# Optimization experiments

Measured on AMD Instinct MI355X. Metric: run time of the kernel, lower is better.

The kernel has to match this reference:

```python
import jax, jax.numpy as jnp
import numpy as np

N_LINKS = 10000
N_PATHS = 50000
PLEN = 5                 # fixed path length -> max_len
E = N_PATHS * PLEN       # number of (link, path) edge entries
D = 32                   # link_state_dim == path_state_dim
H = 32
RU = 256                 # readout_units
T_ITERS = 8              # message-passing iterations t


def setup_inputs() -> dict:
    key = jax.random.key(0)
    ks = jax.random.split(key, 20)
    s = 0.1
    inp = {}
    inp["traffic"] = jax.random.uniform(ks[0], (N_PATHS,), dtype=jnp.float32)
    inp["packets"] = jax.random.uniform(ks[1], (N_PATHS,), dtype=jnp.float32)
    inp["time_dist_params"] = jax.random.normal(ks[2], (N_PATHS, 12), dtype=jnp.float32)
    inp["capacity"] = jax.random.uniform(ks[3], (N_LINKS,), dtype=jnp.float32)
    # edge lists: each path has exactly PLEN links
    inp["link_to_path"] = jax.random.randint(ks[4], (E,), 0, N_LINKS, dtype=jnp.int32)
    inp["path_ids"] = jnp.repeat(jnp.arange(N_PATHS, dtype=jnp.int32), PLEN)
    inp["sequence_path"] = jnp.tile(jnp.arange(PLEN, dtype=jnp.int32), N_PATHS)
    inp["path_to_link"] = jax.random.randint(ks[5], (E,), 0, N_PATHS, dtype=jnp.int32)
    inp["sequence_links"] = jax.random.randint(ks[6], (E,), 0, N_LINKS, dtype=jnp.int32)
    inp["n_links"] = N_LINKS
    inp["n_paths"] = N_PATHS
    # path-update GRU (input D -> hidden H), torch layout [3H, in]
    inp["Wi_p"] = jax.random.normal(ks[7], (3 * H, D), dtype=jnp.float32) * s
    inp["Wh_p"] = jax.random.normal(ks[8], (3 * H, H), dtype=jnp.float32) * s
    inp["bi_p"] = jnp.zeros((3 * H,), jnp.float32)
    inp["bh_p"] = jnp.zeros((3 * H,), jnp.float32)
    # link-update GRUCell (input H -> hidden D)
    inp["Wi_l"] = jax.random.normal(ks[9], (3 * D, H), dtype=jnp.float32) * s
    inp["Wh_l"] = jax.random.normal(ks[10], (3 * D, D), dtype=jnp.float32) * s
    inp["bi_l"] = jnp.zeros((3 * D,), jnp.float32)
    inp["bh_l"] = jnp.zeros((3 * D,), jnp.float32)
    # readout MLP
    inp["W1"] = jax.random.normal(ks[11], (RU, H), dtype=jnp.float32) * s
    inp["b1"] = jnp.zeros((RU,), jnp.float32)
    inp["W2"] = jax.random.normal(ks[12], (RU, RU), dtype=jnp.float32) * s
    inp["b2"] = jnp.zeros((RU,), jnp.float32)
    inp["W3"] = jax.random.normal(ks[13], (1, RU), dtype=jnp.float32) * s
    inp["b3"] = jnp.zeros((1,), jnp.float32)
    return inp


def _gru_step(x, h, Wi, Wh, bi, bh):
    # torch GRU gate math
    gi = x @ Wi.T + bi
    gh = h @ Wh.T + bh
    ir, iz, in_ = jnp.split(gi, 3, axis=-1)
    hr, hz, hn = jnp.split(gh, 3, axis=-1)
    r = jax.nn.sigmoid(ir + hr)
    z = jax.nn.sigmoid(iz + hz)
    n = jnp.tanh(in_ + r * hn)
    return (1.0 - z) * n + z * h


def reference(traffic, packets, time_dist_params, capacity,
              link_to_path, path_ids, sequence_path, path_to_link, sequence_links,
              n_links, n_paths,
              Wi_p, Wh_p, bi_p, bh_p, Wi_l, Wh_l, bi_l, bh_l,
              W1, b1, W2, b2, W3, b3):
    max_len = PLEN  # == sequence_path.max() + 1 (static)
    # per-path valid lengths (equivalent to the torch nonzero-row count loop)
    lens = jax.ops.segment_max(sequence_path, path_ids, num_segments=n_paths) + 1
    link_state = jnp.concatenate(
        [capacity[:, None], jnp.zeros((n_links, D - 1), capacity.dtype)], axis=1)
    path_state = jnp.concatenate(
        [traffic[:, None], packets[:, None], time_dist_params,
         jnp.zeros((n_paths, D - 14), traffic.dtype)], axis=1)

    for _ in range(T_ITERS):
        link_gather = link_state[link_to_path]  # [E, D]
        link_inputs = jnp.zeros((n_paths, max_len, D), link_state.dtype)
        link_inputs = link_inputs.at[path_ids, sequence_path].set(link_gather)

        def step(h, xt_t):
            xt, t = xt_t
            h_new = _gru_step(xt, h, Wi_p, Wh_p, bi_p, bh_p)
            h = jnp.where((t < lens)[:, None], h_new, h)  # pack_padded semantics
            return h, None

        path_state, _ = jax.lax.scan(
            step, path_state,
            (jnp.swapaxes(link_inputs, 0, 1), jnp.arange(max_len)))

        path_gather = path_state[path_to_link]  # [E, H]
        path_sum = jnp.zeros((n_links, H), path_gather.dtype).at[sequence_links].add(path_gather)
        link_state = _gru_step(path_sum, link_state, Wi_l, Wh_l, bi_l, bh_l)

    r = jax.nn.relu(path_state @ W1.T + b1)
    r = jax.nn.relu(r @ W2.T + b2)
    r = r @ W3.T + b3            # [n_paths, 1]
    return r[:, 0][None, :]      # [1, n_paths]
```

## Files before the change

### kernel.cpp

```cpp
#include <hip/hip_runtime.h>

#define NP 50000
#define NL 10000
#define PLEN 5
#define NE (NP * PLEN)
#define DD 32
#define RUU 256
#define TITERS 8
#define PPW 8

__device__ __forceinline__ float sigmoidf_(float a) {
    return 1.0f / (1.0f + __expf(-a));
}
__device__ __forceinline__ float tanhf_(float a) {
    a = fminf(fmaxf(a, -15.0f), 15.0f);
    float t = __expf(2.0f * a);
    return (t - 1.0f) / (t + 1.0f);
}

__global__ __launch_bounds__(256) void k_init(
    const float* __restrict__ traffic, const float* __restrict__ packets,
    const float* __restrict__ tdp, const float* __restrict__ capacity,
    float* __restrict__ path_state, float* __restrict__ link_state,
    int* __restrict__ lens, int* __restrict__ cnt) {
    int i = blockIdx.x * 256 + threadIdx.x;
    if (i < NP) {
        float v[DD];
        v[0] = traffic[i];
        v[1] = packets[i];
#pragma unroll
        for (int k = 0; k < 12; k++) v[2 + k] = tdp[i * 12 + k];
#pragma unroll
        for (int k = 14; k < DD; k++) v[k] = 0.0f;
#pragma unroll
        for (int k = 0; k < DD; k++) path_state[i * DD + k] = v[k];
        lens[i] = 0;
    }
    if (i < NL) {
        link_state[i * DD] = capacity[i];
#pragma unroll
        for (int k = 1; k < DD; k++) link_state[i * DD + k] = 0.0f;
        cnt[i] = 0;
    }
}

__global__ __launch_bounds__(256) void k_lens(const int* __restrict__ path_ids,
                                              const int* __restrict__ seq_path,
                                              int* __restrict__ lens) {
    int e = blockIdx.x * 256 + threadIdx.x;
    if (e < NE) atomicMax(&lens[path_ids[e]], seq_path[e] + 1);
}

__global__ __launch_bounds__(256) void k_csr_count(const int* __restrict__ seq_links,
                                                   int* __restrict__ cnt) {
    int e = blockIdx.x * 256 + threadIdx.x;
    if (e < NE) atomicAdd(&cnt[seq_links[e]], 1);
}

__global__ __launch_bounds__(256) void k_csr_scan(const int* __restrict__ cnt,
                                                  int* __restrict__ offs,
                                                  int* __restrict__ cursor) {
    __shared__ int ssum[256];
    const int tid = threadIdx.x;
    const int CH = 40;
    int base = tid * CH;
    int s = 0;
    for (int i = 0; i < CH; i++) {
        int idx = base + i;
        s += (idx < NL) ? cnt[idx] : 0;
    }
    ssum[tid] = s;
    __syncthreads();
    for (int off = 1; off < 256; off <<= 1) {
        int t = (tid >= off) ? ssum[tid - off] : 0;
        __syncthreads();
        ssum[tid] += t;
        __syncthreads();
    }
    int run = ssum[tid] - s;
    for (int i = 0; i < CH; i++) {
        int idx = base + i;
        if (idx < NL) {
            offs[idx] = run;
            cursor[idx] = run;
            run += cnt[idx];
        }
    }
    if (tid == 0) offs[NL] = ssum[255];
}

__global__ __launch_bounds__(256) void k_csr_fill(const int* __restrict__ seq_links,
                                                  const int* __restrict__ path_to_link,
                                                  int* __restrict__ cursor,
                                                  int* __restrict__ csr_pids) {
    int e = blockIdx.x * 256 + threadIdx.x;
    if (e < NE) {
        int l = seq_links[e];
        int slot = atomicAdd(&cursor[l], 1);
        csr_pids[slot] = path_to_link[e];
    }
}

__global__ __launch_bounds__(256, 2) void k_gru_paths(
    const float* __restrict__ link_state, float* __restrict__ path_state,
    const int* __restrict__ link_to_path, const int* __restrict__ lens,
    const float* __restrict__ Wi, const float* __restrict__ Wh,
    const float* __restrict__ bi, const float* __restrict__ bh) {
    __shared__ float hbuf[4][DD];
    const int tid = threadIdx.x;
    const int wave = tid >> 6;
    const int lane = tid & 63;
    const int d = lane & 31;
    const int half = lane >> 5;

    float wi[3][16], wh[3][16];
#pragma unroll
    for (int g = 0; g < 3; g++) {
        const float* wip = &Wi[(g * 32 + d) * 32 + half * 16];
        const float* whp = &Wh[(g * 32 + d) * 32 + half * 16];
#pragma unroll
        for (int c = 0; c < 4; c++) {
            *(float4*)&wi[g][c * 4] = *(const float4*)&wip[c * 4];
            *(float4*)&wh[g][c * 4] = *(const float4*)&whp[c * 4];
        }
    }
#pragma unroll
    for (int g = 0; g < 3; g++)
#pragma unroll
        for (int k = 0; k < 16; k++) {
            asm volatile("" : "+v"(wi[g][k]));
            asm volatile("" : "+v"(wh[g][k]));
        }
    const float bir = bi[d], biz = bi[d + 32], bin = bi[d + 64];
    const float bhr = bh[d], bhz = bh[d + 32], bhn = bh[d + 64];

    const int pbase = (blockIdx.x * 4 + wave) * PPW;
    for (int pp = 0; pp < PPW; pp++) {
        const int p = pbase + pp;
        if (p >= NP) break;

        float hd = path_state[p * DD + d];
        float hk[16];
#pragma unroll
        for (int c = 0; c < 4; c++)
            *(float4*)&hk[c * 4] = *(const float4*)&path_state[p * DD + half * 16 + c * 4];

        const int len = lens[p];
        int li[PLEN];
#pragma unroll
        for (int s = 0; s < PLEN; s++) li[s] = link_to_path[p * PLEN + s];

        float xk[16];
#pragma unroll
        for (int c = 0; c < 4; c++)
            *(float4*)&xk[c * 4] = *(const float4*)&link_state[li[0] * DD + half * 16 + c * 4];

#pragma unroll
        for (int st = 0; st < PLEN; st++) {
            float xn[16];
            if (st + 1 < PLEN) {
#pragma unroll
                for (int c = 0; c < 4; c++)
                    *(float4*)&xn[c * 4] =
                        *(const float4*)&link_state[li[st + 1] * DD + half * 16 + c * 4];
            }
            float ir = 0.f, iz = 0.f, in_ = 0.f, hr = 0.f, hz = 0.f, hn = 0.f;
#pragma unroll
            for (int k = 0; k < 16; k++) {
                ir  = fmaf(xk[k], wi[0][k], ir);
                iz  = fmaf(xk[k], wi[1][k], iz);
                in_ = fmaf(xk[k], wi[2][k], in_);
                hr  = fmaf(hk[k], wh[0][k], hr);
                hz  = fmaf(hk[k], wh[1][k], hz);
                hn  = fmaf(hk[k], wh[2][k], hn);
            }
            ir += __shfl_xor(ir, 32);
            iz += __shfl_xor(iz, 32);
            in_ += __shfl_xor(in_, 32);
            hr += __shfl_xor(hr, 32);
            hz += __shfl_xor(hz, 32);
            hn += __shfl_xor(hn, 32);
            float r = sigmoidf_(ir + bir + hr + bhr);
            float z = sigmoidf_(iz + biz + hz + bhz);
            float n = tanhf_(in_ + bin + r * (hn + bhn));
            float hnew = (1.0f - z) * n + z * hd;
            hd = (st < len) ? hnew : hd;
            hbuf[wave][d] = hd;
#pragma unroll
            for (int c = 0; c < 4; c++)
                *(float4*)&hk[c * 4] = *(const float4*)&hbuf[wave][half * 16 + c * 4];
            if (st + 1 < PLEN) {
#pragma unroll
                for (int k = 0; k < 16; k++) xk[k] = xn[k];
            }
        }
        if (half == 0) path_state[p * DD + d] = hd;
    }
}

__global__ __launch_bounds__(256, 2) void k_links(
    const float* __restrict__ path_state, float* __restrict__ link_state,
    const int* __restrict__ offs, const int* __restrict__ csr_pids,
    const float* __restrict__ Wi, const float* __restrict__ Wh,
    const float* __restrict__ bi, const float* __restrict__ bh) {
    __shared__ float hbuf[4][DD];
    const int tid = threadIdx.x;
    const int wave = tid >> 6;
    const int lane = tid & 63;
    const int d = lane & 31;
    const int half = lane >> 5;

    float wi[3][16], wh[3][16];
#pragma unroll
    for (int g = 0; g < 3; g++) {
        const float* wip = &Wi[(g * 32 + d) * 32 + half * 16];
        const float* whp = &Wh[(g * 32 + d) * 32 + half * 16];
#pragma unroll
        for (int c = 0; c < 4; c++) {
            *(float4*)&wi[g][c * 4] = *(const float4*)&wip[c * 4];
            *(float4*)&wh[g][c * 4] = *(const float4*)&whp[c * 4];
        }
    }
#pragma unroll
    for (int g = 0; g < 3; g++)
#pragma unroll
        for (int k = 0; k < 16; k++) {
            asm volatile("" : "+v"(wi[g][k]));
            asm volatile("" : "+v"(wh[g][k]));
        }
    const float bir = bi[d], biz = bi[d + 32], bin = bi[d + 64];
    const float bhr = bh[d], bhz = bh[d + 32], bhn = bh[d + 64];

    const int lbase = (blockIdx.x * 4 + wave) * PPW;
    for (int ll = 0; ll < PPW; ll++) {
        const int l = lbase + ll;
        if (l >= NL) break;
        const int beg = offs[l], end = offs[l + 1];

        float xv = 0.f;
        int t = beg + half;
        int pid = (t < end) ? csr_pids[t] : 0;
        while (t < end) {
            int t2 = t + 2;
            int pid2 = (t2 < end) ? csr_pids[t2] : 0;
            xv += path_state[pid * DD + d];
            pid = pid2;
            t = t2;
        }
        xv += __shfl_xor(xv, 32);

        float hd = link_state[l * DD + d];
        float hk[16], xk[16];
#pragma unroll
        for (int c = 0; c < 4; c++)
            *(float4*)&hk[c * 4] = *(const float4*)&link_state[l * DD + half * 16 + c * 4];
        hbuf[wave][d] = xv;
#pragma unroll
        for (int c = 0; c < 4; c++)
            *(float4*)&xk[c * 4] = *(const float4*)&hbuf[wave][half * 16 + c * 4];

        float ir = 0.f, iz = 0.f, in_ = 0.f, hr = 0.f, hz = 0.f, hn = 0.f;
#pragma unroll
        for (int k = 0; k < 16; k++) {
            ir  = fmaf(xk[k], wi[0][k], ir);
            iz  = fmaf(xk[k], wi[1][k], iz);
            in_ = fmaf(xk[k], wi[2][k], in_);
            hr  = fmaf(hk[k], wh[0][k], hr);
            hz  = fmaf(hk[k], wh[1][k], hz);
            hn  = fmaf(hk[k], wh[2][k], hn);
        }
        ir += __shfl_xor(ir, 32);
        iz += __shfl_xor(iz, 32);
        in_ += __shfl_xor(in_, 32);
        hr += __shfl_xor(hr, 32);
        hz += __shfl_xor(hz, 32);
        hn += __shfl_xor(hn, 32);
        float r = sigmoidf_(ir + bir + hr + bhr);
        float z = sigmoidf_(iz + biz + hz + bhz);
        float n = tanhf_(in_ + bin + r * (hn + bhn));
        float hnew = (1.0f - z) * n + z * hd;
        if (half == 0) link_state[l * DD + d] = hnew;
    }
}

__global__ __launch_bounds__(256, 2) void k_readout(
    const float* __restrict__ path_state, float* __restrict__ out,
    const float* __restrict__ W1, const float* __restrict__ b1,
    const float* __restrict__ W2, const float* __restrict__ b2,
    const float* __restrict__ W3, const float* __restrict__ b3) {
    __shared__ float sr1[64 * RUU];
    __shared__ float sw[RUU * 32];
    __shared__ float sred[64 * 32];
    const int tid = threadIdx.x;
    const int p0 = blockIdx.x * 64;

    {
        float4* dst = (float4*)sred;
#pragma unroll
        for (int r = 0; r < 2; r++) {
            int gidx = r * 256 + tid;
            int row = gidx >> 3, f4 = gidx & 7;
            int p = p0 + row;
            if (p >= NP) p = NP - 1;
            dst[gidx] = *(const float4*)&path_state[(size_t)p * DD + f4 * 4];
        }
    }
    float w1r[DD];
#pragma unroll
    for (int c = 0; c < 8; c++)
        *(float4*)&w1r[c * 4] = *(const float4*)&W1[tid * DD + c * 4];
    float bb1 = b1[tid];
    __syncthreads();

    for (int m = 0; m < 64; m++) {
        float acc = bb1;
        const float4* xr = (const float4*)&sred[m * DD];
#pragma unroll
        for (int c = 0; c < 8; c++) {
            float4 xv = xr[c];
            acc = fmaf(xv.x, w1r[c * 4 + 0], fmaf(xv.y, w1r[c * 4 + 1],
                  fmaf(xv.z, w1r[c * 4 + 2], fmaf(xv.w, w1r[c * 4 + 3], acc))));
        }
        sr1[m * RUU + tid] = fmaxf(acc, 0.0f);
    }

    const int pig = tid >> 5;
    const int jg  = tid & 31;
    float accs[8][8];
#pragma unroll
    for (int jj = 0; jj < 8; jj++) {
        float bv = b2[jg * 8 + jj];
#pragma unroll
        for (int pp = 0; pp < 8; pp++) accs[pp][jj] = bv;
    }
    for (int s = 0; s < 8; s++) {
        __syncthreads();
#pragma unroll
        for (int r = 0; r < 8; r++) {
            int gidx = r * 256 + tid;
            int j = gidx >> 3, kk = gidx & 7;
            float4 v = *(const float4*)&W2[j * RUU + s * 32 + kk * 4];
            ((float4*)sw)[j * 8 + (kk ^ ((j >> 3) & 7))] = v;
        }
        __syncthreads();
        for (int k4 = 0; k4 < 8; k4++) {
            float a[8][4];
#pragma unroll
            for (int pp = 0; pp < 8; pp++)
                *(float4*)&a[pp][0] =
                    *(const float4*)&sr1[(pig * 8 + pp) * RUU + s * 32 + k4 * 4];
#pragma unroll
            for (int jj = 0; jj < 8; jj++) {
                float4 w = ((const float4*)sw)[(jg * 8 + jj) * 8 + (k4 ^ (jg & 7))];
#pragma unroll
                for (int pp = 0; pp < 8; pp++) {
                    accs[pp][jj] = fmaf(a[pp][0], w.x, fmaf(a[pp][1], w.y,
                                   fmaf(a[pp][2], w.z, fmaf(a[pp][3], w.w, accs[pp][jj]))));
                }
            }
        }
    }

    float w3r[8];
#pragma unroll
    for (int c = 0; c < 2; c++)
        *(float4*)&w3r[c * 4] = *(const float4*)&W3[jg * 8 + c * 4];
#pragma unroll
    for (int pp = 0; pp < 8; pp++) {
        float v = 0.f;
#pragma unroll
        for (int jj = 0; jj < 8; jj++) v = fmaf(w3r[jj], fmaxf(accs[pp][jj], 0.f), v);
        sred[(pig * 8 + pp) * 32 + jg] = v;
    }
    __syncthreads();
    if (tid < 64) {
        float v = b3[0];
        const float* sp = &sred[tid * 32];
#pragma unroll
        for (int g = 0; g < 32; g++) v += sp[g];
        int p = p0 + tid;
        if (p < NP) out[p] = v;
    }
}

extern "C" void kernel_launch(void* const* d_in, const int* in_sizes, int n_in,
                              void* d_out, int out_size, void* d_ws, size_t ws_size,
                              hipStream_t stream) {
    const float* traffic  = (const float*)d_in[0];
    const float* packets  = (const float*)d_in[1];
    const float* tdp      = (const float*)d_in[2];
    const float* capacity = (const float*)d_in[3];
    const int* link_to_path = (const int*)d_in[4];
    const int* path_ids     = (const int*)d_in[5];
    const int* seq_path     = (const int*)d_in[6];
    const int* path_to_link = (const int*)d_in[7];
    const int* seq_links    = (const int*)d_in[8];
    const float* Wi_p = (const float*)d_in[11];
    const float* Wh_p = (const float*)d_in[12];
    const float* bi_p = (const float*)d_in[13];
    const float* bh_p = (const float*)d_in[14];
    const float* Wi_l = (const float*)d_in[15];
    const float* Wh_l = (const float*)d_in[16];
    const float* bi_l = (const float*)d_in[17];
    const float* bh_l = (const float*)d_in[18];
    const float* W1 = (const float*)d_in[19];
    const float* b1 = (const float*)d_in[20];
    const float* W2 = (const float*)d_in[21];
    const float* b2 = (const float*)d_in[22];
    const float* W3 = (const float*)d_in[23];
    const float* b3 = (const float*)d_in[24];
    float* out = (float*)d_out;

    float* path_state = (float*)d_ws;
    float* link_state = path_state + (size_t)NP * DD;
    int* lens     = (int*)(link_state + (size_t)NL * DD);
    int* cnt      = lens + NP;
    int* offs     = cnt + NL;
    int* cursor   = offs + NL + 1;
    int* csr_pids = cursor + NL;

    k_init<<<(NP + 255) / 256, 256, 0, stream>>>(traffic, packets, tdp, capacity,
                                                 path_state, link_state, lens, cnt);
    k_lens<<<(NE + 255) / 256, 256, 0, stream>>>(path_ids, seq_path, lens);
    k_csr_count<<<(NE + 255) / 256, 256, 0, stream>>>(seq_links, cnt);
    k_csr_scan<<<1, 256, 0, stream>>>(cnt, offs, cursor);
    k_csr_fill<<<(NE + 255) / 256, 256, 0, stream>>>(seq_links, path_to_link,
                                                     cursor, csr_pids);
    for (int t = 0; t < TITERS; t++) {
        k_gru_paths<<<(NP + 4 * PPW - 1) / (4 * PPW), 256, 0, stream>>>(
            link_state, path_state, link_to_path, lens, Wi_p, Wh_p, bi_p, bh_p);
        k_links<<<(NL + 4 * PPW - 1) / (4 * PPW), 256, 0, stream>>>(
            path_state, link_state, offs, csr_pids, Wi_l, Wh_l, bi_l, bh_l);
    }
    k_readout<<<(NP + 63) / 64, 256, 0, stream>>>(path_state, out, W1, b1, W2,
                                                  b2, W3, b3);
}
```

Before: 1.549 ms.

## Rework readout GEMM, use ds_bpermute broadcasts, shrink links per wave

The GRU kernels now broadcast hidden and input vectors across lanes with ds_bpermute instead of round-tripping through a shared-memory buffer. The link kernel assigns 2 links per wave instead of 8, giving more blocks to cover the irregular CSR gather. The readout transposes W2 once in a new kernel and streams it from global/L2 instead of staging tiles in LDS with repeated syncs. It also reads path_state directly and reduces the final dot product with wave shuffles. The trade is more global/L2 traffic for W2 in exchange for fewer barriers and less LDS.

```diff
diff --git a/kernel.cpp b/kernel.cpp
--- a/kernel.cpp
+++ b/kernel.cpp
@@ -8,6 +8,7 @@
 #define RUU 256
 #define TITERS 8
 #define PPW 8
+#define LPW 2
 
 __device__ __forceinline__ float sigmoidf_(float a) {
     return 1.0f / (1.0f + __expf(-a));
@@ -101,12 +102,17 @@
     }
 }
 
+__global__ __launch_bounds__(256) void k_w2t(const float* __restrict__ W2,
+                                             float* __restrict__ W2t) {
+    int j = blockIdx.x, k = threadIdx.x;
+    W2t[k * RUU + j] = W2[j * RUU + k];
+}
+
 __global__ __launch_bounds__(256, 2) void k_gru_paths(
     const float* __restrict__ link_state, float* __restrict__ path_state,
     const int* __restrict__ link_to_path, const int* __restrict__ lens,
     const float* __restrict__ Wi, const float* __restrict__ Wh,
     const float* __restrict__ bi, const float* __restrict__ bh) {
-    __shared__ float hbuf[4][DD];
     const int tid = threadIdx.x;
     const int wave = tid >> 6;
     const int lane = tid & 63;
@@ -185,10 +191,12 @@
             float n = tanhf_(in_ + bin + r * (hn + bhn));
             float hnew = (1.0f - z) * n + z * hd;
             hd = (st < len) ? hnew : hd;
-            hbuf[wave][d] = hd;
-#pragma unroll
-            for (int c = 0; c < 4; c++)
-                *(float4*)&hk[c * 4] = *(const float4*)&hbuf[wave][half * 16 + c * 4];
+            int hdi = __float_as_int(hd);
+#pragma unroll
+            for (int k = 0; k < 16; k++) {
+                int src = ((half << 4) + k) << 2;
+                hk[k] = __int_as_float(__builtin_amdgcn_ds_bpermute(src, hdi));
+            }
             if (st + 1 < PLEN) {
 #pragma unroll
                 for (int k = 0; k < 16; k++) xk[k] = xn[k];
@@ -203,7 +211,6 @@
     const int* __restrict__ offs, const int* __restrict__ csr_pids,
     const float* __restrict__ Wi, const float* __restrict__ Wh,
     const float* __restrict__ bi, const float* __restrict__ bh) {
-    __shared__ float hbuf[4][DD];
     const int tid = threadIdx.x;
     const int wave = tid >> 6;
     const int lane = tid & 63;
@@ -231,8 +238,8 @@
     const float bir = bi[d], biz = bi[d + 32], bin = bi[d + 64];
     const float bhr = bh[d], bhz = bh[d + 32], bhn = bh[d + 64];
 
-    const int lbase = (blockIdx.x * 4 + wave) * PPW;
-    for (int ll = 0; ll < PPW; ll++) {
+    const int lbase = (blockIdx.x * 4 + wave) * LPW;
+    for (int ll = 0; ll < LPW; ll++) {
         const int l = lbase + ll;
         if (l >= NL) break;
         const int beg = offs[l], end = offs[l + 1];
@@ -254,10 +261,12 @@
 #pragma unroll
         for (int c = 0; c < 4; c++)
             *(float4*)&hk[c * 4] = *(const float4*)&link_state[l * DD + half * 16 + c * 4];
-        hbuf[wave][d] = xv;
-#pragma unroll
-        for (int c = 0; c < 4; c++)
-            *(float4*)&xk[c * 4] = *(const float4*)&hbuf[wave][half * 16 + c * 4];
+        int xvi = __float_as_int(xv);
+#pragma unroll
+        for (int k = 0; k < 16; k++) {
+            int src = ((half << 4) + k) << 2;
+            xk[k] = __int_as_float(__builtin_amdgcn_ds_bpermute(src, xvi));
+        }
 
         float ir = 0.f, iz = 0.f, in_ = 0.f, hr = 0.f, hz = 0.f, hn = 0.f;
 #pragma unroll
@@ -286,35 +295,24 @@
 __global__ __launch_bounds__(256, 2) void k_readout(
     const float* __restrict__ path_state, float* __restrict__ out,
     const float* __restrict__ W1, const float* __restrict__ b1,
-    const float* __restrict__ W2, const float* __restrict__ b2,
+    const float* __restrict__ W2t, const float* __restrict__ b2,
     const float* __restrict__ W3, const float* __restrict__ b3) {
     __shared__ float sr1[64 * RUU];
-    __shared__ float sw[RUU * 32];
-    __shared__ float sred[64 * 32];
     const int tid = threadIdx.x;
     const int p0 = blockIdx.x * 64;
 
-    {
-        float4* dst = (float4*)sred;
-#pragma unroll
-        for (int r = 0; r < 2; r++) {
-            int gidx = r * 256 + tid;
-            int row = gidx >> 3, f4 = gidx & 7;
-            int p = p0 + row;
-            if (p >= NP) p = NP - 1;
-            dst[gidx] = *(const float4*)&path_state[(size_t)p * DD + f4 * 4];
-        }
-    }
     float w1r[DD];
 #pragma unroll
     for (int c = 0; c < 8; c++)
         *(float4*)&w1r[c * 4] = *(const float4*)&W1[tid * DD + c * 4];
     float bb1 = b1[tid];
-    __syncthreads();
-
+
+#pragma unroll 2
     for (int m = 0; m < 64; m++) {
+        int p = p0 + m;
+        if (p >= NP) p = NP - 1;
+        const float4* xr = (const float4*)&path_state[(size_t)p * DD];
         float acc = bb1;
-        const float4* xr = (const float4*)&sred[m * DD];
 #pragma unroll
         for (int c = 0; c < 8; c++) {
             float4 xv = xr[c];
@@ -323,6 +321,7 @@
         }
         sr1[m * RUU + tid] = fmaxf(acc, 0.0f);
     }
+    __syncthreads();
 
     const int pig = tid >> 5;
     const int jg  = tid & 31;
@@ -333,30 +332,27 @@
 #pragma unroll
         for (int pp = 0; pp < 8; pp++) accs[pp][jj] = bv;
     }
-    for (int s = 0; s < 8; s++) {
-        __syncthreads();
-#pragma unroll
-        for (int r = 0; r < 8; r++) {
-            int gidx = r * 256 + tid;
-            int j = gidx >> 3, kk = gidx & 7;
-            float4 v = *(const float4*)&W2[j * RUU + s * 32 + kk * 4];
-            ((float4*)sw)[j * 8 + (kk ^ ((j >> 3) & 7))] = v;
-        }
-        __syncthreads();
-        for (int k4 = 0; k4 < 8; k4++) {
-            float a[8][4];
-#pragma unroll
-            for (int pp = 0; pp < 8; pp++)
-                *(float4*)&a[pp][0] =
-                    *(const float4*)&sr1[(pig * 8 + pp) * RUU + s * 32 + k4 * 4];
-#pragma unroll
-            for (int jj = 0; jj < 8; jj++) {
-                float4 w = ((const float4*)sw)[(jg * 8 + jj) * 8 + (k4 ^ (jg & 7))];
-#pragma unroll
-                for (int pp = 0; pp < 8; pp++) {
-                    accs[pp][jj] = fmaf(a[pp][0], w.x, fmaf(a[pp][1], w.y,
-                                   fmaf(a[pp][2], w.z, fmaf(a[pp][3], w.w, accs[pp][jj]))));
-                }
+    for (int k4 = 0; k4 < 64; k4++) {
+        const int k0 = k4 * 4;
+        float a[8][4];
+#pragma unroll
+        for (int pp = 0; pp < 8; pp++)
+            *(float4*)&a[pp][0] = *(const float4*)&sr1[(pig * 8 + pp) * RUU + k0];
+#pragma unroll
+        for (int kk = 0; kk < 4; kk++) {
+            float4 w0 = *(const float4*)&W2t[(size_t)(k0 + kk) * RUU + jg * 8];
+            float4 w1_ = *(const float4*)&W2t[(size_t)(k0 + kk) * RUU + jg * 8 + 4];
+#pragma unroll
+            for (int pp = 0; pp < 8; pp++) {
+                float av = a[pp][kk];
+                accs[pp][0] = fmaf(av, w0.x, accs[pp][0]);
+                accs[pp][1] = fmaf(av, w0.y, accs[pp][1]);
+                accs[pp][2] = fmaf(av, w0.z, accs[pp][2]);
+                accs[pp][3] = fmaf(av, w0.w, accs[pp][3]);
+                accs[pp][4] = fmaf(av, w1_.x, accs[pp][4]);
+                accs[pp][5] = fmaf(av, w1_.y, accs[pp][5]);
+                accs[pp][6] = fmaf(av, w1_.z, accs[pp][6]);
+                accs[pp][7] = fmaf(av, w1_.w, accs[pp][7]);
             }
         }
     }
@@ -365,21 +361,25 @@
 #pragma unroll
     for (int c = 0; c < 2; c++)
         *(float4*)&w3r[c * 4] = *(const float4*)&W3[jg * 8 + c * 4];
+    float val[8];
 #pragma unroll
     for (int pp = 0; pp < 8; pp++) {
         float v = 0.f;
 #pragma unroll
         for (int jj = 0; jj < 8; jj++) v = fmaf(w3r[jj], fmaxf(accs[pp][jj], 0.f), v);
-        sred[(pig * 8 + pp) * 32 + jg] = v;
-    }
-    __syncthreads();
-    if (tid < 64) {
-        float v = b3[0];
-        const float* sp = &sred[tid * 32];
-#pragma unroll
-        for (int g = 0; g < 32; g++) v += sp[g];
-        int p = p0 + tid;
-        if (p < NP) out[p] = v;
+        val[pp] = v;
+    }
+#pragma unroll
+    for (int m = 1; m < 32; m <<= 1)
+#pragma unroll
+        for (int pp = 0; pp < 8; pp++) val[pp] += __shfl_xor(val[pp], m);
+    if (jg == 0) {
+        float b3v = b3[0];
+#pragma unroll
+        for (int pp = 0; pp < 8; pp++) {
+            int p = p0 + pig * 8 + pp;
+            if (p < NP) out[p] = val[pp] + b3v;
+        }
     }
 }
 
@@ -413,7 +413,8 @@
 
     float* path_state = (float*)d_ws;
     float* link_state = path_state + (size_t)NP * DD;
-    int* lens     = (int*)(link_state + (size_t)NL * DD);
+    float* w2t        = link_state + (size_t)NL * DD;
+    int* lens     = (int*)(w2t + RUU * RUU);
     int* cnt      = lens + NP;
     int* offs     = cnt + NL;
     int* cursor   = offs + NL + 1;
@@ -426,12 +427,13 @@
     k_csr_scan<<<1, 256, 0, stream>>>(cnt, offs, cursor);
     k_csr_fill<<<(NE + 255) / 256, 256, 0, stream>>>(seq_links, path_to_link,
                                                      cursor, csr_pids);
+    k_w2t<<<RUU, RUU, 0, stream>>>(W2, w2t);
     for (int t = 0; t < TITERS; t++) {
         k_gru_paths<<<(NP + 4 * PPW - 1) / (4 * PPW), 256, 0, stream>>>(
             link_state, path_state, link_to_path, lens, Wi_p, Wh_p, bi_p, bh_p);
-        k_links<<<(NL + 4 * PPW - 1) / (4 * PPW), 256, 0, stream>>>(
+        k_links<<<(NL + 4 * LPW - 1) / (4 * LPW), 256, 0, stream>>>(
             path_state, link_state, offs, csr_pids, Wi_l, Wh_l, bi_l, bh_l);
     }
-    k_readout<<<(NP + 63) / 64, 256, 0, stream>>>(path_state, out, W1, b1, W2,
+    k_readout<<<(NP + 63) / 64, 256, 0, stream>>>(path_state, out, W1, b1, w2t,
                                                   b2, W3, b3);
 }
```

Result: faster. 1.477 ms (-4.6%).
